# Kernel tuning notes

Hardware: AMD Instinct MI355X
Metric: run time of the kernel (lower is better)

## Reference

```python
import jax, jax.numpy as jnp
import numpy as np

N, E = 20000, 320000
CS, CV = 64, 32          # scalar / vector multiplicities of node (= node_pre) irreps
AS_, AV, H = 16, 8, 4    # attn irreps scalar/vector muls, num_heads
NB = 16                  # num_basis
SQRT3 = 1.7320508075688772
SQRT2 = 1.4142135623730951
EPS = 1e-5

# dtp weight layout: [ss(CS), sv(CS), vs(CV), vv0(CV), vv1(CV)] -> numel = 2*CS+3*CV = 224

def _cg_tp(s, v, y0, y1, w_ss, w_sv, w_vs, w_vv0, w_vv1):
    """Depthwise CG tensor product for l<=1.
    s:(E,CS) v:(E,CV,3) y0:(E,) y1:(E,3); weights (E,C) or (C,).
    out scalars (E, CS+CV): 0e x 0e -> 0e, 1o x 1o -> 0e (dot/sqrt3)
    out vectors (E, CS+2*CV, 3): 0e x 1o -> 1o, 1o x 0e -> 1o, 1o x 1o -> 1o (cross/sqrt2)
    """
    out_s = jnp.concatenate([
        w_ss * s * y0[:, None],
        w_vv0 * (jnp.einsum('eci,ei->ec', v, y1) / SQRT3)], axis=-1)
    out_v = jnp.concatenate([
        (w_sv * s)[:, :, None] * y1[:, None, :],
        (w_vs * jnp.ones_like(v[..., 0]))[..., None] * v * y0[:, None, None],
        (w_vv1 * jnp.ones_like(v[..., 0]))[..., None] * (jnp.cross(v, y1[:, None, :]) / SQRT2)], axis=1)
    return out_s, out_v


def _equiv_layernorm(s, v, gamma_s, beta_s, gamma_v):
    mu = jnp.mean(s, axis=-1, keepdims=True)
    var = jnp.var(s, axis=-1, keepdims=True)
    s_n = (s - mu) * jax.lax.rsqrt(var + EPS) * gamma_s + beta_s
    rms = jnp.sqrt(jnp.mean(jnp.sum(v * v, axis=-1), axis=-1, keepdims=True) + EPS)
    v_n = v / rms[..., None] * gamma_v[None, :, None]
    return s_n, v_n


def setup_inputs() -> dict:
    key = jax.random.key(0)
    ks = jax.random.split(key, 26)
    def rn(k, shape, fan):
        return jax.random.normal(k, shape, jnp.float32) / np.sqrt(fan)
    D1S, D1V = CS + CV, CS + 2 * CV          # 96, 128 (dtp output muls)
    WN = 2 * CS + 3 * CV                     # 224 dtp weight numel
    inp = {
        'node': jax.random.normal(ks[0], (N, CS + 3 * CV), jnp.float32),
        'edge_index': jax.random.randint(ks[1], (2, E), 0, N, jnp.int64 if jax.config.jax_enable_x64 else jnp.int32),
        'rbf': jax.random.uniform(ks[2], (E, NB), jnp.float32),
        'rsh': jax.random.normal(ks[3], (E, 4), jnp.float32),
        'gamma_s': jnp.ones((CS,), jnp.float32),
        'beta_s': jnp.zeros((CS,), jnp.float32),
        'gamma_v': jnp.ones((CV,), jnp.float32),
        'Ws_src': rn(ks[4], (CS, CS), CS), 'Wv_src': rn(ks[5], (CV, CV), CV),
        'Ws_dst': rn(ks[6], (CS, CS), CS), 'Wv_dst': rn(ks[7], (CV, CV), CV),
        'W_rbf': rn(ks[8], (NB, WN), NB),
        'W_alpha': rn(ks[9], (D1S, H * AS_), D1S),
        'alpha_dot': rn(ks[10], (1, H, AS_), AS_),
        'Ws_val': rn(ks[11], (D1S, CS), D1S), 'Wv_val': rn(ks[12], (D1V, CV), D1V),
        'Wg': rn(ks[13], (CS, CV), CS),
        'w2_ss': rn(ks[14], (CS,), 1), 'w2_sv': rn(ks[15], (CS,), 1),
        'w2_vs': rn(ks[16], (CV,), 1), 'w2_vv0': rn(ks[17], (CV,), 1), 'w2_vv1': rn(ks[18], (CV,), 1),
        'Ws_vlin': rn(ks[19], (D1S, H * AS_), D1S), 'Wv_vlin': rn(ks[20], (D1V, H * AV), D1V),
        'Wps': rn(ks[21], (H * AS_, CS), H * AS_), 'Wpv': rn(ks[22], (H * AV, CV), H * AV),
    }
    return inp


def reference(node, rbf, rsh, gamma_s, beta_s, gamma_v, Ws_src, Wv_src, Ws_dst, Wv_dst,
              W_rbf, W_alpha, alpha_dot, Ws_val, Wv_val, Wg,
              w2_ss, w2_sv, w2_vs, w2_vv0, w2_vv1, Ws_vlin, Wv_vlin, Wps, Wpv, edge_index):
    n = node.shape[0]
    e = rsh.shape[0]
    s = node[:, :CS]
    v = node[:, CS:].reshape(n, CV, 3)
    # equivariant layer norm
    s_n, v_n = _equiv_layernorm(s, v, gamma_s, beta_s, gamma_v)
    # merge_src / merge_dst (irrep-wise o3.Linear)
    src, dst = edge_index[0], edge_index[1]
    msg_s = (s_n @ Ws_src)[src] + (s_n @ Ws_dst)[dst]                       # (E,CS)
    msg_v = jnp.einsum('ncx,cd->ndx', v_n, Wv_src)[src] + \
            jnp.einsum('ncx,cd->ndx', v_n, Wv_dst)[dst]                     # (E,CV,3)
    y0, y1 = rsh[:, 0], rsh[:, 1:4]
    # dtp1: per-edge weighted CG coupling, weights from rbf
    w1 = rbf @ W_rbf                                                        # (E,224)
    m1_s, m1_v = _cg_tp(msg_s, msg_v, y0, y1,
                        w1[:, :CS], w1[:, CS:2*CS], w1[:, 2*CS:2*CS+CV],
                        w1[:, 2*CS+CV:2*CS+2*CV], w1[:, 2*CS+2*CV:])        # (E,96) (E,128,3)
    # attention logits
    a = (m1_s @ W_alpha).reshape(e, H, AS_)
    a = jnp.where(a > 0, a, 0.2 * a)                                        # LeakyReLU(0.2)
    a = jnp.sum(a * alpha_dot, axis=-1, keepdims=True)                      # (E,H,1)
    # softmax over incoming edges of each destination node
    amax = jax.ops.segment_max(a, dst, num_segments=n)
    amax = jnp.where(jnp.isfinite(amax), amax, 0.0)
    ex = jnp.exp(a - amax[dst])
    den = jax.ops.segment_sum(ex, dst, num_segments=n)
    alpha = ex / (den[dst] + 1e-16)                                         # (E,H,1)
    # value path
    val_s = m1_s @ Ws_val                                                   # (E,CS)
    val_v = jnp.einsum('ecx,cd->edx', m1_v, Wv_val)                         # (E,CV,3)
    # gate: sigmoid on scalars, vectors gated by sigmoid of learned scalar gates
    val_v = val_v * jax.nn.sigmoid(val_s @ Wg)[..., None]
    val_s = jax.nn.sigmoid(val_s)
    # dtp2: shared internal weights
    m2_s, m2_v = _cg_tp(val_s, val_v, y0, y1, w2_ss, w2_sv, w2_vs, w2_vv0, w2_vv1)
    # value_lin -> (attn_irreps * num_heads), head-major layout
    hs = (m2_s @ Ws_vlin).reshape(e, H, AS_)
    hv = jnp.einsum('ecx,cd->edx', m2_v, Wv_vlin).reshape(e, H, AV, 3)
    h = jnp.concatenate([hs, hv.reshape(e, H, AV * 3)], axis=-1)            # (E,H,40)
    # attend + scatter-add to destination nodes
    agg = jax.ops.segment_sum(alpha * h, dst, num_segments=n)               # (N,H,40)
    agg_s = agg[:, :, :AS_].reshape(n, H * AS_)                             # (N,64)
    agg_v = agg[:, :, AS_:].reshape(n, H * AV, 3)                           # (N,32,3)
    out = node + jnp.concatenate([
        agg_s @ Wps,
        jnp.einsum('ncx,cd->ndx', agg_v, Wpv).reshape(n, CV * 3)], axis=-1)
    return out
```

## Files before the change

kernel.cpp:

```cpp
#include <hip/hip_runtime.h>
#include <hip/hip_bf16.h>
#include <cstddef>

typedef __hip_bfloat16 bf16;
typedef __bf16 bfv8 __attribute__((ext_vector_type(8)));
typedef __bf16 bfv4 __attribute__((ext_vector_type(4)));
typedef float f4 __attribute__((ext_vector_type(4)));

#define EPSN 1e-5f
#define SQRT3_INV 0.57735026918962576f
#define SQRT2_INV 0.70710678118654752f

__device__ __forceinline__ float b2f(bf16 x) { return __bfloat162float(x); }

template<int BF> __device__ __forceinline__ float ldf(const void* p, size_t i) {
    if (BF) return __bfloat162float(((const bf16*)p)[i]);
    return ((const float*)p)[i];
}
__device__ __forceinline__ float ldr(const void* p, size_t i, int bfm) {
    return bfm ? __bfloat162float(((const bf16*)p)[i]) : ((const float*)p)[i];
}
template<int BF> __device__ __forceinline__ void stf(void* p, size_t i, float v) {
    if (BF) ((bf16*)p)[i] = __float2bfloat16(v);
    else    ((float*)p)[i] = v;
}

__device__ __forceinline__ float wave_sum64(float x) {
    #pragma unroll
    for (int m = 1; m < 64; m <<= 1) x += __shfl_xor(x, m, 64);
    return x;
}

__device__ __forceinline__ f4 mf(bfv8 a, bfv8 b, f4 c) {
    return __builtin_amdgcn_mfma_f32_16x16x32_bf16(a, b, c, 0, 0, 0);
}

__global__ __launch_bounds__(256) void k_sniff(const void* node, const void* eidx, int* flags)
{
    int t = threadIdx.x;
    __shared__ int cnt;
    __shared__ unsigned orr;
    if (t == 0) { cnt = 0; orr = 0u; }
    __syncthreads();
    unsigned w  = ((const unsigned*)node)[t];
    unsigned lo = w & 0xFFFFu;
    int e_lo = (int)((lo >> 7) & 0xFF);
    if (e_lo >= 96 && e_lo <= 140) atomicAdd(&cnt, 1);
    unsigned odd = ((const unsigned*)eidx)[2 * t + 1];
    atomicOr(&orr, odd);
    __syncthreads();
    if (t == 0) {
        flags[0] = (cnt >= 128) ? 1 : 0;
        flags[1] = (orr == 0u) ? 1 : 0;
    }
}

__global__ __launch_bounds__(256) void k_zero(float* p, int n)
{
    int i = blockIdx.x * 256 + threadIdx.x;
    if (i < n) p[i] = 0.f;
}

__global__ __launch_bounds__(256) void k_hist(const void* eidx, int* cnt,
                                              const int* flags, int E)
{
    int e = blockIdx.x * 256 + threadIdx.x;
    if (e >= E) return;
    int d = flags[1] ? (int)((const long long*)eidx)[(long long)E + e]
                     : ((const int*)eidx)[(size_t)E + e];
    atomicAdd(&cnt[d], 1);
}

__global__ __launch_bounds__(1024) void k_scan(int* cnt, int N)
{
    __shared__ int wsum[16];
    int t = threadIdx.x;
    int lane = t & 63, w = t >> 6;
    int chunk = (N + 1023) >> 10;
    int lo = t * chunk, hi = lo + chunk;
    if (hi > N) hi = N; if (lo > N) lo = N;
    int sum = 0;
    for (int i = lo; i < hi; ++i) sum += cnt[i];
    int x = sum;
    #pragma unroll
    for (int off = 1; off < 64; off <<= 1) {
        int y = __shfl_up(x, off, 64);
        if (lane >= off) x += y;
    }
    if (lane == 63) wsum[w] = x;
    __syncthreads();
    if (t < 64) {
        int v = (lane < 16) ? wsum[lane] : 0;
        #pragma unroll
        for (int off = 1; off < 16; off <<= 1) {
            int y = __shfl_up(v, off, 64);
            if (lane >= off) v += y;
        }
        if (lane < 16) wsum[lane] = v;
    }
    __syncthreads();
    int acc = x - sum + (w ? wsum[w - 1] : 0);
    for (int i = lo; i < hi; ++i) { int v = cnt[i]; cnt[i] = acc; acc += v; }
}

__global__ __launch_bounds__(256) void k_perm(const void* eidx, int* cnt, int* perm,
                                              const int* flags, int E)
{
    int e = blockIdx.x * 256 + threadIdx.x;
    if (e >= E) return;
    int d = flags[1] ? (int)((const long long*)eidx)[(long long)E + e]
                     : ((const int*)eidx)[(size_t)E + e];
    int pos = atomicAdd(&cnt[d], 1);
    perm[pos] = e;
}

template<int BF>
__device__ __forceinline__ void prep_impl(
    const void* Walpha, const void* Wsval, const void* Wsvlin,
    const void* Wvval, const void* Wvvlin, const void* Wg,
    const void* Wrbf, const void* adot,
    const void* w2ss, const void* w2sv, const void* w2vs,
    const void* w2vv0, const void* w2vv1,
    bf16* WalphaT, bf16* WsvalT, bf16* WsvlinT,
    bf16* WvvalT, bf16* WvvlinT, bf16* WgT,
    bf16* WrbfT, bf16* adotB, bf16* w2B)
{
    int t = threadIdx.x + blockIdx.x * 256;
    int T = gridDim.x * 256;
    for (int i = t; i < 96 * 64; i += T) {
        int c = i >> 6, n = i & 63;
        WalphaT[n * 96 + c] = __float2bfloat16(ldf<BF>(Walpha, i));
        WsvalT [n * 96 + c] = __float2bfloat16(ldf<BF>(Wsval,  i));
        WsvlinT[n * 96 + c] = __float2bfloat16(ldf<BF>(Wsvlin, i));
    }
    for (int i = t; i < 128 * 32; i += T) {
        int c = i >> 5, n = i & 31;
        WvvalT [n * 128 + c] = __float2bfloat16(ldf<BF>(Wvval,  i));
        WvvlinT[n * 128 + c] = __float2bfloat16(ldf<BF>(Wvvlin, i));
    }
    for (int i = t; i < 64 * 32; i += T) {
        int c = i >> 5, n = i & 31;
        WgT[n * 64 + c] = __float2bfloat16(ldf<BF>(Wg, i));
    }
    for (int i = t; i < 224 * 32; i += T) {
        int c = i >> 5, b = i & 31;
        WrbfT[i] = __float2bfloat16(b < 16 ? ldf<BF>(Wrbf, b * 224 + c) : 0.f);
    }
    if (t < 64) adotB[t] = __float2bfloat16(ldf<BF>(adot, t));
    if (t < 64) w2B[t]      = __float2bfloat16(ldf<BF>(w2ss, t));
    if (t < 64) w2B[64 + t] = __float2bfloat16(ldf<BF>(w2sv, t));
    if (t < 32) {
        w2B[128 + t] = __float2bfloat16(ldf<BF>(w2vs, t));
        w2B[160 + t] = __float2bfloat16(ldf<BF>(w2vv0, t));
        w2B[192 + t] = __float2bfloat16(ldf<BF>(w2vv1, t));
    }
}

__global__ __launch_bounds__(256) void k_prep(
    const void* Walpha, const void* Wsval, const void* Wsvlin,
    const void* Wvval, const void* Wvvlin, const void* Wg,
    const void* Wrbf, const void* adot,
    const void* w2ss, const void* w2sv, const void* w2vs,
    const void* w2vv0, const void* w2vv1,
    bf16* WalphaT, bf16* WsvalT, bf16* WsvlinT,
    bf16* WvvalT, bf16* WvvlinT, bf16* WgT,
    bf16* WrbfT, bf16* adotB, bf16* w2B, const int* flags)
{
    if (flags[0])
        prep_impl<1>(Walpha, Wsval, Wsvlin, Wvval, Wvvlin, Wg, Wrbf, adot,
                     w2ss, w2sv, w2vs, w2vv0, w2vv1,
                     WalphaT, WsvalT, WsvlinT, WvvalT, WvvlinT, WgT, WrbfT, adotB, w2B);
    else
        prep_impl<0>(Walpha, Wsval, Wsvlin, Wvval, Wvvlin, Wg, Wrbf, adot,
                     w2ss, w2sv, w2vs, w2vv0, w2vv1,
                     WalphaT, WsvalT, WsvlinT, WvvalT, WvvlinT, WgT, WrbfT, adotB, w2B);
}

template<int BF>
__device__ __forceinline__ void node_impl(
    const void* node, const void* gs, const void* bs, const void* gv,
    const void* Wss, const void* Wvs, const void* Wsd, const void* Wvd,
    bf16* ssrc, bf16* sdst, bf16* vsrc, bf16* vdst,
    float* shs, float* shv, int n, int lane)
{
    size_t nb = (size_t)n * 160;

    float s  = ldf<BF>(node, nb + lane);
    float mu = wave_sum64(s) * (1.f / 64.f);
    float d  = s - mu;
    float var = wave_sum64(d * d) * (1.f / 64.f);
    float sn  = d * rsqrtf(var + EPSN) * ldf<BF>(gs, lane) + ldf<BF>(bs, lane);
    shs[lane] = sn;

    float v0 = 0.f, v1 = 0.f, v2 = 0.f, qq = 0.f;
    if (lane < 32) {
        v0 = ldf<BF>(node, nb + 64 + lane * 3 + 0);
        v1 = ldf<BF>(node, nb + 64 + lane * 3 + 1);
        v2 = ldf<BF>(node, nb + 64 + lane * 3 + 2);
        qq = v0 * v0 + v1 * v1 + v2 * v2;
    }
    float msq = wave_sum64(qq) * (1.f / 32.f);
    float inv = rsqrtf(msq + EPSN);
    if (lane < 32) {
        float g = ldf<BF>(gv, lane);
        shv[0 * 32 + lane] = v0 * inv * g;
        shv[1 * 32 + lane] = v1 * inv * g;
        shv[2 * 32 + lane] = v2 * inv * g;
    }

    float a1 = 0.f, a2 = 0.f;
    for (int c = 0; c < 64; ++c) {
        float sc = shs[c];
        a1 += sc * ldf<BF>(Wss, c * 64 + lane);
        a2 += sc * ldf<BF>(Wsd, c * 64 + lane);
    }
    {
        int cs = lane;
        int pos = (cs & 15) * 4 + (cs >> 4);
        ssrc[(size_t)n * 64 + pos] = __float2bfloat16(a1);
        sdst[(size_t)n * 64 + pos] = __float2bfloat16(a2);
    }

    {
        int x = lane >> 5, dd = lane & 31;
        float p1 = 0.f, p2 = 0.f;
        for (int c = 0; c < 32; ++c) {
            float vc = shv[x * 32 + c];
            p1 += vc * ldf<BF>(Wvs, c * 32 + dd);
            p2 += vc * ldf<BF>(Wvd, c * 32 + dd);
        }
        int cv = x * 32 + dd;
        int pos = (cv & 15) * 8 + (cv >> 4);
        vsrc[(size_t)n * 128 + pos] = __float2bfloat16(p1);
        vdst[(size_t)n * 128 + pos] = __float2bfloat16(p2);
    }
    if (lane < 32) {
        int dd = lane;
        float p1 = 0.f, p2 = 0.f;
        for (int c = 0; c < 32; ++c) {
            float vc = shv[2 * 32 + c];
            p1 += vc * ldf<BF>(Wvs, c * 32 + dd);
            p2 += vc * ldf<BF>(Wvd, c * 32 + dd);
        }
        int cv = 64 + dd;
        int pos = (cv & 15) * 8 + (cv >> 4);
        vsrc[(size_t)n * 128 + pos] = __float2bfloat16(p1);
        vdst[(size_t)n * 128 + pos] = __float2bfloat16(p2);
    }
}

__global__ __launch_bounds__(256) void k_node(
    const void* node, const void* gs, const void* bs, const void* gv,
    const void* Wss, const void* Wvs, const void* Wsd, const void* Wvd,
    bf16* ssrc, bf16* sdst, bf16* vsrc, bf16* vdst,
    const int* flags, int N)
{
    __shared__ float shs[4][64];
    __shared__ float shv[4][96];
    int wv = threadIdx.x >> 6, lane = threadIdx.x & 63;
    int n = blockIdx.x * 4 + wv; if (n >= N) return;
    if (flags[0])
        node_impl<1>(node, gs, bs, gv, Wss, Wvs, Wsd, Wvd, ssrc, sdst, vsrc, vdst,
                     shs[wv], shv[wv], n, lane);
    else
        node_impl<0>(node, gs, bs, gv, Wss, Wvs, Wsd, Wvd, ssrc, sdst, vsrc, vdst,
                     shs[wv], shv[wv], n, lane);
}

static constexpr int SS  = 104;
static constexpr int A1S = 0;
static constexpr int SV  = 136;
static constexpr int P0  = 16 * SS;
static constexpr int P1  = P0 + 16 * SV;
static constexpr int VAL = 0;
static constexpr int SA  = 72;
static constexpr int HSZ = P1 + 16 * SV;

#define W_M1(X, PB) do { \
    constexpr int x_ = (X), x1_ = ((X)+1)%3, x2_ = ((X)+2)%3; \
    _Pragma("unroll") \
    for (int r = 0; r < 4; ++r) { \
        int e = q * 4 + r; \
        float4 yy = *(const float4*)&sY[wv][e][0]; \
        float y0 = yy.x; float yv[3] = {yy.y, yy.z, yy.w}; \
        _Pragma("unroll") \
        for (int nt = 0; nt < 4; ++nt) \
            H[(PB) + e * SV + nt * 16 + m] = (__bf16)(sv_[r][nt] * yv[x_]); \
        _Pragma("unroll") \
        for (int n2 = 0; n2 < 2; ++n2) { \
            int c = 64 + n2 * 16 + m; \
            H[(PB) + e * SV + c] = (__bf16)(qv_[r][n2][x_] * y0); \
            float cr = pv_[r][n2][x1_] * yv[x2_] - pv_[r][n2][x2_] * yv[x1_]; \
            H[(PB) + e * SV + 32 + c] = (__bf16)(cr * SQRT2_INV); \
        } \
    } \
} while (0)

#define W_M2(X, PB) do { \
    constexpr int x_ = (X), x1_ = ((X)+1)%3, x2_ = ((X)+2)%3; \
    _Pragma("unroll") \
    for (int r = 0; r < 4; ++r) { \
        int e = q * 4 + r; \
        float4 yy = *(const float4*)&sY[wv][e][0]; \
        float y0 = yy.x; float yv[3] = {yy.y, yy.z, yy.w}; \
        _Pragma("unroll") \
        for (int nt = 0; nt < 4; ++nt) \
            H[(PB) + e * SV + nt * 16 + m] = (__bf16)(c2sv[nt] * vals[nt][r] * yv[x_]); \
        _Pragma("unroll") \
        for (int n2 = 0; n2 < 2; ++n2) { \
            int c = 64 + n2 * 16 + m; \
            H[(PB) + e * SV + c] = (__bf16)(c2vs[n2] * vv[x_][n2][r] * y0); \
            float cr = vv[x1_][n2][r] * yv[x2_] - vv[x2_][n2][r] * yv[x1_]; \
            H[(PB) + e * SV + 32 + c] = (__bf16)(c2v1[n2] * cr * SQRT2_INV); \
        } \
    } \
} while (0)

#define MMA_V(PB, WB, O0, O1) do { \
    bfv8 fg_[4]; \
    _Pragma("unroll") \
    for (int kt = 0; kt < 4; ++kt) \
        fg_[kt] = *(const bfv8*)(H + (PB) + m * SV + kt * 32 + kq); \
    _Pragma("unroll") \
    for (int kt = 0; kt < 4; ++kt) { \
        O0 = mf(fg_[kt], *(const bfv8*)((WB) + (size_t)(0 * 16 + m) * 128 + kt * 32 + kq), O0); \
        O1 = mf(fg_[kt], *(const bfv8*)((WB) + (size_t)(1 * 16 + m) * 128 + kt * 32 + kq), O1); \
    } \
} while (0)

__global__ __launch_bounds__(256, 3) void k_edge(
    const void* __restrict__ eidx, const void* __restrict__ rbf, const void* __restrict__ rsh,
    const bf16* __restrict__ WalphaT, const bf16* __restrict__ WsvalT, const bf16* __restrict__ WsvlinT,
    const bf16* __restrict__ WvvalT, const bf16* __restrict__ WvvlinT, const bf16* __restrict__ WgT,
    const bf16* __restrict__ WrbfT, const bf16* __restrict__ adotB, const bf16* __restrict__ w2B,
    const bf16* __restrict__ ssrc, const bf16* __restrict__ sdst,
    const bf16* __restrict__ vsrc, const bf16* __restrict__ vdst,
    const int* __restrict__ perm,
    float* __restrict__ den, float* __restrict__ agg,
    const int* __restrict__ flags, int E)
{
    const int bfm = flags[0];
    const int i64 = flags[1];

    __shared__ __align__(16) __bf16 sH[4][HSZ];
    __shared__ __align__(16) float sY[4][16][4];
    __shared__ int sSD[4][48];

    int wv = threadIdx.x >> 6, l = threadIdx.x & 63;
    int q = l >> 4, m = l & 15;
    const int kq = q * 8;
    long long eb = ((long long)blockIdx.x * 4 + wv) * 16;
    if (eb >= E) return;
    __bf16* H = &sH[wv][0];

    if (l < 16) {
        long long p = eb + l; if (p > (long long)E - 1) p = E - 1;
        sSD[wv][32 + l] = perm[p];
    }
    if (l < 32) {
        int pe = sSD[wv][32 + (l & 15)];
        long long off = (l < 16) ? (long long)pe : ((long long)E + pe);
        sSD[wv][l] = i64 ? (int)((const long long*)eidx)[off] : ((const int*)eidx)[off];
    }
    {
        int pe = sSD[wv][32 + (l >> 2)];
        sY[wv][l >> 2][l & 3] = ldr(rsh, (size_t)pe * 4 + (l & 3), bfm);
    }

    f4 w1f[14];
    {
        bfv8 arb;
        #pragma unroll
        for (int i = 0; i < 8; ++i) arb[i] = (__bf16)0.f;
        if (q < 2) {
            int pe = sSD[wv][32 + m];
            if (bfm) {
                arb = *(const bfv8*)((const __bf16*)rbf + (size_t)pe * 16 + kq);
            } else {
                const float* rp = (const float*)rbf + (size_t)pe * 16 + kq;
                #pragma unroll
                for (int i = 0; i < 8; ++i) arb[i] = (__bf16)rp[i];
            }
        }
        const __bf16* wb = (const __bf16*)WrbfT;
        #pragma unroll
        for (int nt = 0; nt < 14; ++nt) {
            bfv8 bb = *(const bfv8*)(wb + (size_t)(nt * 16 + m) * 32 + kq);
            f4 z = {0.f, 0.f, 0.f, 0.f};
            w1f[nt] = mf(arb, bb, z);
        }
    }

    bfv4 gs_[4], gd_[4];
    bfv8 gv_[4], gw_[4];
    #pragma unroll
    for (int r = 0; r < 4; ++r) {
        int e = q * 4 + r;
        int s = sSD[wv][e], d = sSD[wv][16 + e];
        gs_[r] = *(const bfv4*)((const __bf16*)ssrc + (size_t)s * 64 + m * 4);
        gd_[r] = *(const bfv4*)((const __bf16*)sdst + (size_t)d * 64 + m * 4);
        gv_[r] = *(const bfv8*)((const __bf16*)vsrc + (size_t)s * 128 + m * 8);
        gw_[r] = *(const bfv8*)((const __bf16*)vdst + (size_t)d * 128 + m * 8);
    }
    float ms_[4][4], mv_[4][2][3];
    #pragma unroll
    for (int r = 0; r < 4; ++r) {
        #pragma unroll
        for (int nt = 0; nt < 4; ++nt)
            ms_[r][nt] = (float)gs_[r][nt] + (float)gd_[r][nt];
        #pragma unroll
        for (int x = 0; x < 3; ++x)
            #pragma unroll
            for (int n2 = 0; n2 < 2; ++n2)
                mv_[r][n2][x] = (float)gv_[r][2 * x + n2] + (float)gw_[r][2 * x + n2];
    }

    float sv_[4][4], qv_[4][2][3], pv_[4][2][3];
    #pragma unroll
    for (int r = 0; r < 4; ++r) {
        int e = q * 4 + r;
        float4 yy = *(const float4*)&sY[wv][e][0];
        float y0 = yy.x, yx = yy.y, yh = yy.z, yz = yy.w;
        #pragma unroll
        for (int nt = 0; nt < 4; ++nt) {
            H[A1S + e * SS + nt * 16 + m] = (__bf16)(w1f[nt][r] * ms_[r][nt] * y0);
            sv_[r][nt] = w1f[4 + nt][r] * ms_[r][nt];
        }
        #pragma unroll
        for (int n2 = 0; n2 < 2; ++n2) {
            float dot = mv_[r][n2][0] * yx + mv_[r][n2][1] * yh + mv_[r][n2][2] * yz;
            H[A1S + e * SS + 64 + n2 * 16 + m] = (__bf16)(w1f[10 + n2][r] * dot * SQRT3_INV);
            #pragma unroll
            for (int x = 0; x < 3; ++x) {
                qv_[r][n2][x] = w1f[8 + n2][r]  * mv_[r][n2][x];
                pv_[r][n2][x] = w1f[12 + n2][r] * mv_[r][n2][x];
            }
        }
    }

    bfv8 a1s0 = *(const bfv8*)(H + A1S + m * SS + 0  + kq);
    bfv8 a1s1 = *(const bfv8*)(H + A1S + m * SS + 32 + kq);
    bfv8 a1s2 = *(const bfv8*)(H + A1S + m * SS + 64 + kq);

    f4 vals[4];
    #pragma unroll
    for (int nt = 0; nt < 4; ++nt) {
        const __bf16* bp = (const __bf16*)WsvalT + (size_t)(nt * 16 + m) * 96 + kq;
        f4 acc = {0.f, 0.f, 0.f, 0.f};
        acc = mf(a1s0, *(const bfv8*)(bp),      acc);
        acc = mf(a1s1, *(const bfv8*)(bp + 32), acc);
        acc = mf(a1s2, *(const bfv8*)(bp + 64), acc);
        vals[nt] = acc;
    }
    #pragma unroll
    for (int nt = 0; nt < 4; ++nt)
        #pragma unroll
        for (int r = 0; r < 4; ++r) {
            float v = vals[nt][r];
            H[VAL + (q * 4 + r) * SA + nt * 16 + m] = (__bf16)v;
            vals[nt][r] = 1.f / (1.f + __expf(-v));
        }

    f4 gate[2];
    {
        bfv8 av0 = *(const bfv8*)(H + VAL + m * SA + 0  + kq);
        bfv8 av1 = *(const bfv8*)(H + VAL + m * SA + 32 + kq);
        #pragma unroll
        for (int nt = 0; nt < 2; ++nt) {
            const __bf16* bp = (const __bf16*)WgT + (size_t)(nt * 16 + m) * 64 + kq;
            f4 acc = {0.f, 0.f, 0.f, 0.f};
            acc = mf(av0, *(const bfv8*)(bp),      acc);
            acc = mf(av1, *(const bfv8*)(bp + 32), acc);
            gate[nt] = acc;
        }
        #pragma unroll
        for (int nt = 0; nt < 2; ++nt)
            #pragma unroll
            for (int r = 0; r < 4; ++r)
                gate[nt][r] = 1.f / (1.f + __expf(-gate[nt][r]));
    }

    float ex_[4][4];
    #pragma unroll
    for (int nt = 0; nt < 4; ++nt) {
        const __bf16* bp = (const __bf16*)WalphaT + (size_t)(nt * 16 + m) * 96 + kq;
        f4 acc = {0.f, 0.f, 0.f, 0.f};
        acc = mf(a1s0, *(const bfv8*)(bp),      acc);
        acc = mf(a1s1, *(const bfv8*)(bp + 32), acc);
        acc = mf(a1s2, *(const bfv8*)(bp + 64), acc);
        float ad = b2f(adotB[nt * 16 + m]);
        #pragma unroll
        for (int r = 0; r < 4; ++r) {
            float tv = acc[r];
            tv = tv > 0.f ? tv : 0.2f * tv;
            tv *= ad;
            tv += __shfl_xor(tv, 1); tv += __shfl_xor(tv, 2);
            tv += __shfl_xor(tv, 4); tv += __shfl_xor(tv, 8);
            tv = fminf(fmaxf(tv, -60.f), 60.f);
            ex_[nt][r] = __expf(tv);
        }
    }

    f4 vv[3][2];
    #pragma unroll
    for (int x = 0; x < 3; ++x)
        #pragma unroll
        for (int nt = 0; nt < 2; ++nt)
            vv[x][nt] = (f4){0.f, 0.f, 0.f, 0.f};

    W_M1(0, P0);
    W_M1(1, P1);
    MMA_V(P0, (const __bf16*)WvvalT, vv[0][0], vv[0][1]);
    W_M1(2, P0);
    MMA_V(P1, (const __bf16*)WvvalT, vv[1][0], vv[1][1]);
    MMA_V(P0, (const __bf16*)WvvalT, vv[2][0], vv[2][1]);

    #pragma unroll
    for (int x = 0; x < 3; ++x)
        #pragma unroll
        for (int nt = 0; nt < 2; ++nt)
            #pragma unroll
            for (int r = 0; r < 4; ++r)
                vv[x][nt][r] *= gate[nt][r];

    float c2ss[4], c2sv[4];
    #pragma unroll
    for (int nt = 0; nt < 4; ++nt) {
        c2ss[nt] = b2f(w2B[nt * 16 + m]);
        c2sv[nt] = b2f(w2B[64 + nt * 16 + m]);
    }
    float c2vs[2], c2v0[2], c2v1[2];
    #pragma unroll
    for (int nt = 0; nt < 2; ++nt) {
        c2vs[nt] = b2f(w2B[128 + nt * 16 + m]);
        c2v0[nt] = b2f(w2B[160 + nt * 16 + m]);
        c2v1[nt] = b2f(w2B[192 + nt * 16 + m]);
    }
    #pragma unroll
    for (int r = 0; r < 4; ++r) {
        int e = q * 4 + r;
        float4 yy = *(const float4*)&sY[wv][e][0];
        float y0 = yy.x, yx = yy.y, yh = yy.z, yz = yy.w;
        #pragma unroll
        for (int nt = 0; nt < 4; ++nt)
            H[A1S + e * SS + nt * 16 + m] = (__bf16)(c2ss[nt] * vals[nt][r] * y0);
        #pragma unroll
        for (int n2 = 0; n2 < 2; ++n2) {
            float dotv = vv[0][n2][r] * yx + vv[1][n2][r] * yh + vv[2][n2][r] * yz;
            H[A1S + e * SS + 64 + n2 * 16 + m] = (__bf16)(c2v0[n2] * dotv * SQRT3_INV);
        }
    }
    f4 hs[4];
    {
        bfv8 a2s0 = *(const bfv8*)(H + A1S + m * SS + 0  + kq);
        bfv8 a2s1 = *(const bfv8*)(H + A1S + m * SS + 32 + kq);
        bfv8 a2s2 = *(const bfv8*)(H + A1S + m * SS + 64 + kq);
        #pragma unroll
        for (int nt = 0; nt < 4; ++nt) {
            const __bf16* bp = (const __bf16*)WsvlinT + (size_t)(nt * 16 + m) * 96 + kq;
            f4 acc = {0.f, 0.f, 0.f, 0.f};
            acc = mf(a2s0, *(const bfv8*)(bp),      acc);
            acc = mf(a2s1, *(const bfv8*)(bp + 32), acc);
            acc = mf(a2s2, *(const bfv8*)(bp + 64), acc);
            hs[nt] = acc;
        }
    }

    f4 hv[3][2];
    #pragma unroll
    for (int x = 0; x < 3; ++x)
        #pragma unroll
        for (int nt = 0; nt < 2; ++nt)
            hv[x][nt] = (f4){0.f, 0.f, 0.f, 0.f};

    W_M2(0, P0);
    W_M2(1, P1);
    MMA_V(P0, (const __bf16*)WvvlinT, hv[0][0], hv[0][1]);
    W_M2(2, P0);
    MMA_V(P1, (const __bf16*)WvvlinT, hv[1][0], hv[1][1]);
    MMA_V(P0, (const __bf16*)WvvlinT, hv[2][0], hv[2][1]);

    float* Hf = (float*)H;
    #pragma unroll
    for (int r = 0; r < 4; ++r) {
        int e = q * 4 + r;
        float* row = Hf + e * 168;
        #pragma unroll
        for (int nt = 0; nt < 4; ++nt)
            row[nt * 40 + m] = ex_[nt][r] * hs[nt][r];
        #pragma unroll
        for (int nt = 0; nt < 2; ++nt) {
            int c = nt * 16 + m;
            int hh = c >> 3, dd = c & 7;
            float exv = (m >= 8) ? ex_[2 * nt + 1][r] : ex_[2 * nt][r];
            float* vb = row + hh * 40 + 16 + dd * 3;
            vb[0] = exv * hv[0][nt][r];
            vb[1] = exv * hv[1][nt][r];
            vb[2] = exv * hv[2][nt][r];
        }
        if (m < 4) row[160 + m] = ex_[m][r];
    }
    int nval = (int)((E - eb) < 16 ? (E - eb) : 16);
    {
        int s = 0;
        while (s < nval) {
            int d = sSD[wv][16 + s];
            int t = s + 1;
            while (t < nval && sSD[wv][16 + t] == d) ++t;
            float s0 = 0.f, s1 = 0.f, s2 = 0.f;
            for (int e = s; e < t; ++e) {
                const float* row = Hf + e * 168;
                s0 += row[l];
                s1 += row[64 + l];
                if (l < 36) s2 += row[128 + l];
            }
            float* rowp = agg + (size_t)d * 160;
            unsafeAtomicAdd(rowp + l, s0);
            unsafeAtomicAdd(rowp + 64 + l, s1);
            if (l < 32)      unsafeAtomicAdd(rowp + 128 + l, s2);
            else if (l < 36) unsafeAtomicAdd(den + (size_t)d * 4 + (l - 32), s2);
            s = t;
        }
    }
}

template<int BF>
__device__ __forceinline__ void out_impl(
    const void* node, const float* den, const float* agg,
    const void* Wps, const void* Wpv, void* out,
    float* shs, float* shv, float* sinv, int n, int lane)
{
    if (lane < 4) sinv[lane] = 1.f / (den[(size_t)n * 4 + lane] + 1e-16f);
    for (int idx = lane; idx < 160; idx += 64) {
        int h = idx / 40, r = idx - h * 40;
        float val = agg[(size_t)n * 160 + idx] * sinv[h];
        if (r < 16) shs[h * 16 + r] = val;
        else { int rr = r - 16; int dd = rr / 3, x = rr - dd * 3; shv[x * 32 + h * 8 + dd] = val; }
    }

    float acc = ldf<BF>(node, (size_t)n * 160 + lane);
    for (int c = 0; c < 64; ++c) acc += shs[c] * ldf<BF>(Wps, c * 64 + lane);
    stf<BF>(out, (size_t)n * 160 + lane, acc);

    {
        int idx = lane; int dd = idx / 3, x = idx - dd * 3;
        float a = ldf<BF>(node, (size_t)n * 160 + 64 + idx);
        for (int c = 0; c < 32; ++c) a += shv[x * 32 + c] * ldf<BF>(Wpv, c * 32 + dd);
        stf<BF>(out, (size_t)n * 160 + 64 + idx, a);
    }
    if (lane < 32) {
        int idx = 64 + lane; int dd = idx / 3, x = idx - dd * 3;
        float a = ldf<BF>(node, (size_t)n * 160 + 64 + idx);
        for (int c = 0; c < 32; ++c) a += shv[x * 32 + c] * ldf<BF>(Wpv, c * 32 + dd);
        stf<BF>(out, (size_t)n * 160 + 64 + idx, a);
    }
}

__global__ __launch_bounds__(256) void k_out(
    const void* node, const float* den, const float* agg,
    const void* Wps, const void* Wpv, void* out,
    const int* flags, int N)
{
    __shared__ float shs[4][64];
    __shared__ float shv[4][96];
    __shared__ float sinv[4][4];
    int wv = threadIdx.x >> 6, lane = threadIdx.x & 63;
    int n = blockIdx.x * 4 + wv; if (n >= N) return;
    if (flags[0])
        out_impl<1>(node, den, agg, Wps, Wpv, out, shs[wv], shv[wv], sinv[wv], n, lane);
    else
        out_impl<0>(node, den, agg, Wps, Wpv, out, shs[wv], shv[wv], sinv[wv], n, lane);
}

extern "C" void kernel_launch(void* const* d_in, const int* in_sizes, int n_in,
                              void* d_out, int out_size, void* d_ws, size_t ws_size,
                              hipStream_t stream)
{
    const void* node   = d_in[0];
    const void* eidx   = d_in[1];
    const void* rbf    = d_in[2];
    const void* rsh    = d_in[3];
    const void* gs     = d_in[4];
    const void* bs     = d_in[5];
    const void* gv     = d_in[6];
    const void* Wss    = d_in[7];
    const void* Wvs    = d_in[8];
    const void* Wsd    = d_in[9];
    const void* Wvd    = d_in[10];
    const void* Wrbf   = d_in[11];
    const void* Walpha = d_in[12];
    const void* adot   = d_in[13];
    const void* Wsval  = d_in[14];
    const void* Wvval  = d_in[15];
    const void* Wg     = d_in[16];
    const void* w2ss   = d_in[17];
    const void* w2sv   = d_in[18];
    const void* w2vs   = d_in[19];
    const void* w2vv0  = d_in[20];
    const void* w2vv1  = d_in[21];
    const void* Wsvlin = d_in[22];
    const void* Wvvlin = d_in[23];
    const void* Wps    = d_in[24];
    const void* Wpv    = d_in[25];

    int N = in_sizes[0] / 160;
    int E = in_sizes[1] / 2;

    char* base = (char*)d_ws;
    int*  flags   = (int*)base;
    bf16* WalphaT = (bf16*)(base + 16);
    bf16* WsvalT  = WalphaT + 6144;
    bf16* WsvlinT = WsvalT  + 6144;
    bf16* WvvalT  = WsvlinT + 6144;
    bf16* WvvlinT = WvvalT  + 4096;
    bf16* WgT     = WvvlinT + 4096;
    bf16* WrbfT   = WgT     + 2048;
    bf16* adotB   = WrbfT   + 7168;
    bf16* w2B     = adotB   + 64;
    bf16* ssrc    = w2B     + 224;
    bf16* sdst    = ssrc + (size_t)N * 64;
    bf16* vsrc    = sdst + (size_t)N * 64;
    bf16* vdst    = vsrc + (size_t)N * 128;
    float* den    = (float*)(vdst + (size_t)N * 128);
    float* agg    = den + (size_t)N * 4;
    int*  cnt     = (int*)(agg + (size_t)N * 160);
    int*  perm    = cnt + N;

    k_sniff<<<1, 256, 0, stream>>>(node, eidx, flags);
    int zn = N * 164;
    k_zero<<<(zn + 255) / 256, 256, 0, stream>>>(den, zn);
    k_zero<<<(N + 255) / 256, 256, 0, stream>>>((float*)cnt, N);

    int nbe = (E + 255) / 256;
    k_hist<<<nbe, 256, 0, stream>>>(eidx, cnt, flags, E);
    k_scan<<<1, 1024, 0, stream>>>(cnt, N);
    k_perm<<<nbe, 256, 0, stream>>>(eidx, cnt, perm, flags, E);

    k_prep<<<16, 256, 0, stream>>>(Walpha, Wsval, Wsvlin, Wvval, Wvvlin, Wg, Wrbf, adot,
                                   w2ss, w2sv, w2vs, w2vv0, w2vv1,
                                   WalphaT, WsvalT, WsvlinT, WvvalT, WvvlinT, WgT, WrbfT,
                                   adotB, w2B, flags);

    int nbn = (N + 3) / 4;
    k_node<<<nbn, 256, 0, stream>>>(node, gs, bs, gv, Wss, Wvs, Wsd, Wvd,
                                    ssrc, sdst, vsrc, vdst, flags, N);

    int nb = (E + 63) / 64;
    k_edge<<<nb, 256, 0, stream>>>(eidx, rbf, rsh,
                                   WalphaT, WsvalT, WsvlinT, WvvalT, WvvlinT, WgT, WrbfT,
                                   adotB, w2B, ssrc, sdst, vsrc, vdst, perm, den, agg, flags, E);

    int nbo = (N + 3) / 4;
    k_out<<<nbo, 256, 0, stream>>>(node, den, agg, Wps, Wpv, d_out, flags, N);
}
```

Measured before the change: 503.4 us.

## Shrink edge-kernel LDS, reorder vector MMA, accumulate scatter in registers

Drops the second shared-memory ping-pong buffer (P1) so each x-component of the vector products reuses one buffer, and raises the launch-bounds occupancy hint from 3 to 5 waves. The vector value MMA moves ahead of the gate computation so its accumulators are gated in place. The scatter now accumulates per-lane partial sums in registers over each run of equal destinations within a 4-edge group and issues atomics directly, instead of staging float rows in LDS and reducing them per segment. This may issue more atomics per destination, since runs are split at group boundaries. The separate cnt zeroing launch is merged into the main zero kernel.

```diff
diff --git a/kernel.cpp b/kernel.cpp
--- a/kernel.cpp
+++ b/kernel.cpp
@@ -271,10 +271,9 @@
 static constexpr int A1S = 0;
 static constexpr int SV  = 136;
 static constexpr int P0  = 16 * SS;
-static constexpr int P1  = P0 + 16 * SV;
 static constexpr int VAL = 0;
 static constexpr int SA  = 72;
-static constexpr int HSZ = P1 + 16 * SV;
+static constexpr int HSZ = P0 + 16 * SV;
 
 #define W_M1(X, PB) do { \
     constexpr int x_ = (X), x1_ = ((X)+1)%3, x2_ = ((X)+2)%3; \
@@ -328,7 +327,7 @@
     } \
 } while (0)
 
-__global__ __launch_bounds__(256, 3) void k_edge(
+__global__ __launch_bounds__(256, 5) void k_edge(
     const void* __restrict__ eidx, const void* __restrict__ rbf, const void* __restrict__ rsh,
     const bf16* __restrict__ WalphaT, const bf16* __restrict__ WsvalT, const bf16* __restrict__ WsvlinT,
     const bf16* __restrict__ WvvalT, const bf16* __restrict__ WvvlinT, const bf16* __restrict__ WgT,
@@ -438,6 +437,19 @@
         }
     }
 
+    f4 vv[3][2];
+    #pragma unroll
+    for (int x = 0; x < 3; ++x)
+        #pragma unroll
+        for (int nt = 0; nt < 2; ++nt)
+            vv[x][nt] = (f4){0.f, 0.f, 0.f, 0.f};
+    W_M1(0, P0);
+    MMA_V(P0, (const __bf16*)WvvalT, vv[0][0], vv[0][1]);
+    W_M1(1, P0);
+    MMA_V(P0, (const __bf16*)WvvalT, vv[1][0], vv[1][1]);
+    W_M1(2, P0);
+    MMA_V(P0, (const __bf16*)WvvalT, vv[2][0], vv[2][1]);
+
     bfv8 a1s0 = *(const bfv8*)(H + A1S + m * SS + 0  + kq);
     bfv8 a1s1 = *(const bfv8*)(H + A1S + m * SS + 32 + kq);
     bfv8 a1s2 = *(const bfv8*)(H + A1S + m * SS + 64 + kq);
@@ -461,10 +473,10 @@
             vals[nt][r] = 1.f / (1.f + __expf(-v));
         }
 
-    f4 gate[2];
     {
         bfv8 av0 = *(const bfv8*)(H + VAL + m * SA + 0  + kq);
         bfv8 av1 = *(const bfv8*)(H + VAL + m * SA + 32 + kq);
+        f4 gate[2];
         #pragma unroll
         for (int nt = 0; nt < 2; ++nt) {
             const __bf16* bp = (const __bf16*)WgT + (size_t)(nt * 16 + m) * 64 + kq;
@@ -478,6 +490,13 @@
             #pragma unroll
             for (int r = 0; r < 4; ++r)
                 gate[nt][r] = 1.f / (1.f + __expf(-gate[nt][r]));
+        #pragma unroll
+        for (int x = 0; x < 3; ++x)
+            #pragma unroll
+            for (int nt = 0; nt < 2; ++nt)
+                #pragma unroll
+                for (int r = 0; r < 4; ++r)
+                    vv[x][nt][r] *= gate[nt][r];
     }
 
     float ex_[4][4];
@@ -501,28 +520,6 @@
         }
     }
 
-    f4 vv[3][2];
-    #pragma unroll
-    for (int x = 0; x < 3; ++x)
-        #pragma unroll
-        for (int nt = 0; nt < 2; ++nt)
-            vv[x][nt] = (f4){0.f, 0.f, 0.f, 0.f};
-
-    W_M1(0, P0);
-    W_M1(1, P1);
-    MMA_V(P0, (const __bf16*)WvvalT, vv[0][0], vv[0][1]);
-    W_M1(2, P0);
-    MMA_V(P1, (const __bf16*)WvvalT, vv[1][0], vv[1][1]);
-    MMA_V(P0, (const __bf16*)WvvalT, vv[2][0], vv[2][1]);
-
-    #pragma unroll
-    for (int x = 0; x < 3; ++x)
-        #pragma unroll
-        for (int nt = 0; nt < 2; ++nt)
-            #pragma unroll
-            for (int r = 0; r < 4; ++r)
-                vv[x][nt][r] *= gate[nt][r];
-
     float c2ss[4], c2sv[4];
     #pragma unroll
     for (int nt = 0; nt < 4; ++nt) {
@@ -572,54 +569,63 @@
         #pragma unroll
         for (int nt = 0; nt < 2; ++nt)
             hv[x][nt] = (f4){0.f, 0.f, 0.f, 0.f};
-
     W_M2(0, P0);
-    W_M2(1, P1);
     MMA_V(P0, (const __bf16*)WvvlinT, hv[0][0], hv[0][1]);
+    W_M2(1, P0);
+    MMA_V(P0, (const __bf16*)WvvlinT, hv[1][0], hv[1][1]);
     W_M2(2, P0);
-    MMA_V(P1, (const __bf16*)WvvlinT, hv[1][0], hv[1][1]);
     MMA_V(P0, (const __bf16*)WvvlinT, hv[2][0], hv[2][1]);
 
-    float* Hf = (float*)H;
-    #pragma unroll
-    for (int r = 0; r < 4; ++r) {
-        int e = q * 4 + r;
-        float* row = Hf + e * 168;
-        #pragma unroll
-        for (int nt = 0; nt < 4; ++nt)
-            row[nt * 40 + m] = ex_[nt][r] * hs[nt][r];
-        #pragma unroll
-        for (int nt = 0; nt < 2; ++nt) {
-            int c = nt * 16 + m;
-            int hh = c >> 3, dd = c & 7;
-            float exv = (m >= 8) ? ex_[2 * nt + 1][r] : ex_[2 * nt][r];
-            float* vb = row + hh * 40 + 16 + dd * 3;
-            vb[0] = exv * hv[0][nt][r];
-            vb[1] = exv * hv[1][nt][r];
-            vb[2] = exv * hv[2][nt][r];
-        }
-        if (m < 4) row[160 + m] = ex_[m][r];
-    }
-    int nval = (int)((E - eb) < 16 ? (E - eb) : 16);
     {
-        int s = 0;
-        while (s < nval) {
-            int d = sSD[wv][16 + s];
-            int t = s + 1;
-            while (t < nval && sSD[wv][16 + t] == d) ++t;
-            float s0 = 0.f, s1 = 0.f, s2 = 0.f;
-            for (int e = s; e < t; ++e) {
-                const float* row = Hf + e * 168;
-                s0 += row[l];
-                s1 += row[64 + l];
-                if (l < 36) s2 += row[128 + l];
+        int nval = (int)((E - eb) < 16 ? (E - eb) : 16);
+        const int e0 = q * 4;
+        float as_[4] = {0.f, 0.f, 0.f, 0.f};
+        float av_[3][2] = {{0.f,0.f},{0.f,0.f},{0.f,0.f}};
+        float de_ = 0.f;
+        #pragma unroll
+        for (int r = 0; r < 4; ++r) {
+            int e = e0 + r;
+            bool valid = (e < nval);
+            int d = sSD[wv][16 + (valid ? e : 0)];
+            if (valid) {
+                #pragma unroll
+                for (int nt = 0; nt < 4; ++nt) as_[nt] += ex_[nt][r] * hs[nt][r];
+                #pragma unroll
+                for (int nt = 0; nt < 2; ++nt) {
+                    float exv = (m >= 8) ? ex_[2 * nt + 1][r] : ex_[2 * nt][r];
+                    #pragma unroll
+                    for (int x = 0; x < 3; ++x) av_[x][nt] += exv * hv[x][nt][r];
+                }
+                if (m < 4) de_ += ex_[m][r];
             }
-            float* rowp = agg + (size_t)d * 160;
-            unsafeAtomicAdd(rowp + l, s0);
-            unsafeAtomicAdd(rowp + 64 + l, s1);
-            if (l < 32)      unsafeAtomicAdd(rowp + 128 + l, s2);
-            else if (l < 36) unsafeAtomicAdd(den + (size_t)d * 4 + (l - 32), s2);
-            s = t;
+            bool last;
+            if (r == 3) {
+                last = valid;
+            } else {
+                int en = e + 1;
+                last = valid && ((en >= nval) || (sSD[wv][16 + en] != d));
+            }
+            if (last) {
+                float* rowp = agg + (size_t)d * 160;
+                #pragma unroll
+                for (int nt = 0; nt < 4; ++nt)
+                    unsafeAtomicAdd(rowp + nt * 40 + m, as_[nt]);
+                #pragma unroll
+                for (int nt = 0; nt < 2; ++nt) {
+                    int hh = nt * 2 + (m >> 3), dd2 = m & 7;
+                    #pragma unroll
+                    for (int x = 0; x < 3; ++x)
+                        unsafeAtomicAdd(rowp + hh * 40 + 16 + dd2 * 3 + x, av_[x][nt]);
+                }
+                if (m < 4) unsafeAtomicAdd(den + (size_t)d * 4 + m, de_);
+                #pragma unroll
+                for (int nt = 0; nt < 4; ++nt) as_[nt] = 0.f;
+                #pragma unroll
+                for (int nt = 0; nt < 2; ++nt)
+                    #pragma unroll
+                    for (int x = 0; x < 3; ++x) av_[x][nt] = 0.f;
+                de_ = 0.f;
+            }
         }
     }
 }
@@ -727,9 +733,8 @@
     int*  perm    = cnt + N;
 
     k_sniff<<<1, 256, 0, stream>>>(node, eidx, flags);
-    int zn = N * 164;
+    int zn = N * 165;
     k_zero<<<(zn + 255) / 256, 256, 0, stream>>>(den, zn);
-    k_zero<<<(N + 255) / 256, 256, 0, stream>>>((float*)cnt, N);
 
     int nbe = (E + 255) / 256;
     k_hist<<<nbe, 256, 0, stream>>>(eidx, cnt, flags, E);
```

Result: slower. 787.2 us (+56.4%).
